# Performance work log

Measured on AMD Instinct MI355X. Metric: run time of the kernel, lower is better.

Reference implementation:

```python
import jax, jax.numpy as jnp
import numpy as np

B, TQ, TK, DQ, DK = 8, 2048, 2048, 512, 512


def setup_inputs() -> dict:
    key = jax.random.key(0)
    kq, kk, kv, km, kw = jax.random.split(key, 5)
    q = jax.random.normal(kq, (B, TQ, DQ), dtype=jnp.float32)
    k = jax.random.normal(kk, (B, TK, DK), dtype=jnp.float32)
    v = jax.random.normal(kv, (B, TK, DK), dtype=jnp.float32)
    attn_mask = jax.random.randint(km, (B, TQ, TK), 0, 2) > 0
    # xavier_uniform for (DQ, DK)
    limit = float(np.sqrt(6.0 / (DQ + DK)))
    weights = jax.random.uniform(kw, (DQ, DK), minval=-limit, maxval=limit, dtype=jnp.float32)
    return {"q": q, "k": k, "v": v, "attn_mask": attn_mask, "weights": weights}


def reference(q, k, v, attn_mask, weights):
    # scores: (B, TQ, TK) = (q @ W) @ k^T
    qw = jnp.einsum('bqd,de->bqe', q, weights)
    scores = jnp.einsum('bqe,bke->bqk', qw, k)
    scores = jnp.where(attn_mask, -jnp.inf, scores)
    attention = jax.nn.softmax(scores, axis=-1)
    # dropout_rate = 0.0 -> identity
    output = jnp.einsum('bqk,bkd->bqd', attention, v)
    return (output, attention)
```

## Files before the change

### kernel.cpp

```cpp
#include <hip/hip_runtime.h>
#include <stdint.h>

#define TQs 2048
#define TKs 2048
#define DDs 512
#define NBs 8

typedef float f32x4 __attribute__((ext_vector_type(4)));
typedef short bf16x8 __attribute__((ext_vector_type(8)));
typedef short bf16x4 __attribute__((ext_vector_type(4)));

__device__ __forceinline__ unsigned short f2bf(float x){
  unsigned u = __float_as_uint(x);
  return (unsigned short)((u + 0x7fffu + ((u>>16)&1u)) >> 16);
}
__device__ __forceinline__ float bf2f(unsigned short h){
  return __uint_as_float(((unsigned)h)<<16);
}

__device__ __forceinline__ void gload16(const void* g, void* l){
  __builtin_amdgcn_global_load_lds(
      (const __attribute__((address_space(1))) unsigned int*)(unsigned long long)(uintptr_t)g,
      (__attribute__((address_space(3))) unsigned int*)(unsigned int)(uintptr_t)l,
      16, 0, 0);
}

__global__ __launch_bounds__(256) void k0_split_k(const float* __restrict__ kk,
                                                  short* __restrict__ kh, short* __restrict__ kl){
  const long n4 = (long)NBs*TKs*DDs/4;
  for(long i = (long)blockIdx.x*256 + threadIdx.x; i < n4; i += (long)gridDim.x*256){
    f32x4 x = ((const f32x4*)kk)[i];
    bf16x4 h, l;
    #pragma unroll
    for(int j=0;j<4;j++){
      unsigned short hj = f2bf(x[j]);
      h[j] = (short)hj;
      l[j] = (short)f2bf(x[j] - bf2f(hj));
    }
    ((bf16x4*)kh)[i] = h;
    ((bf16x4*)kl)[i] = l;
  }
}

__global__ __launch_bounds__(256) void k0_transpose_v(const float* __restrict__ v, short* __restrict__ vt){
  __shared__ float tile[64][65];
  int b = blockIdx.z;
  int t0 = blockIdx.x*64, d0 = blockIdx.y*64;
  int tid = threadIdx.x;
  int r = tid>>2, cs = (tid&3)*16;
  const float* src = v + ((long)b*TKs + t0 + r)*DDs + d0 + cs;
  #pragma unroll
  for(int i=0;i<4;i++){
    f32x4 x = ((const f32x4*)src)[i];
    tile[r][cs+4*i+0]=x[0]; tile[r][cs+4*i+1]=x[1]; tile[r][cs+4*i+2]=x[2]; tile[r][cs+4*i+3]=x[3];
  }
  __syncthreads();
  int dr = tid>>2, ts = (tid&3)*16;
  bf16x8 b0, b1;
  #pragma unroll
  for(int i=0;i<8;i++){ b0[i] = (short)f2bf(tile[ts+i][dr]); b1[i] = (short)f2bf(tile[ts+8+i][dr]); }
  short* dst = vt + ((long)b*DDs + d0 + dr)*TKs + t0 + ts;
  ((bf16x8*)dst)[0] = b0;
  ((bf16x8*)dst)[1] = b1;
}

__global__ __launch_bounds__(256) void k0_wt(const float* __restrict__ wsrc,
                                             short* __restrict__ wth, short* __restrict__ wtl){
  __shared__ float tile[64][65];
  int d0 = blockIdx.x*64, e0 = blockIdx.y*64;
  int tid = threadIdx.x;
  int r = tid>>2, cs = (tid&3)*16;
  const float* src = wsrc + ((long)(d0 + r))*DDs + e0 + cs;
  #pragma unroll
  for(int i=0;i<4;i++){
    f32x4 x = ((const f32x4*)src)[i];
    tile[r][cs+4*i+0]=x[0]; tile[r][cs+4*i+1]=x[1]; tile[r][cs+4*i+2]=x[2]; tile[r][cs+4*i+3]=x[3];
  }
  __syncthreads();
  int er = tid>>2, ds = (tid&3)*16;
  bf16x8 h0,h1,l0,l1;
  #pragma unroll
  for(int i=0;i<8;i++){
    float x = tile[ds+i][er];
    unsigned short hh = f2bf(x);
    h0[i] = (short)hh; l0[i] = (short)f2bf(x - bf2f(hh));
  }
  #pragma unroll
  for(int i=0;i<8;i++){
    float x = tile[ds+8+i][er];
    unsigned short hh = f2bf(x);
    h1[i] = (short)hh; l1[i] = (short)f2bf(x - bf2f(hh));
  }
  short* dh = wth + ((long)(e0+er))*DDs + d0 + ds;
  short* dl = wtl + ((long)(e0+er))*DDs + d0 + ds;
  ((bf16x8*)dh)[0] = h0; ((bf16x8*)dh)[1] = h1;
  ((bf16x8*)dl)[0] = l0; ((bf16x8*)dl)[1] = l1;
}

__global__ __launch_bounds__(256,2) void k1_qw(const float* __restrict__ q,
                                               const short* __restrict__ wth, const short* __restrict__ wtl,
                                               short* __restrict__ qwh, short* __restrict__ qwl){
  __shared__ short qah[8192], qal[8192];
  __shared__ short wbh[8192], wbl[8192];
  int q0 = blockIdx.x*128, e0 = blockIdx.y*128;
  int tid = threadIdx.x, lane = tid&63, w4 = tid>>6;
  int wm = w4>>1, wn = w4&1;
  int i15 = lane&15, g4 = lane>>4;
  f32x4 acc[4][4];
  #pragma unroll
  for(int a=0;a<4;a++)
    #pragma unroll
    for(int bq=0;bq<4;bq++) acc[a][bq] = (f32x4){0.f,0.f,0.f,0.f};
  for(int k0=0;k0<DDs;k0+=64){
    __syncthreads();
    #pragma unroll
    for(int j=0;j<4;j++){
      int J = j*4 + w4;
      long so = (long)(e0 + (J>>1)*16 + i15)*DDs + k0 + ((J&1)*4 + g4)*8;
      gload16(wth + so, &wbh[J*512]);
      gload16(wtl + so, &wbl[J*512]);
    }
    #pragma unroll
    for(int j=0;j<4;j++){
      int c = j*256 + tid;
      int ci = c&15, cg = (c>>4)&3, cks = (c>>6)&1, crb = c>>7;
      const float* s = q + (long)(q0 + crb*16 + ci)*DDs + k0 + (cks*4+cg)*8;
      f32x4 x0 = ((const f32x4*)s)[0];
      f32x4 x1 = ((const f32x4*)s)[1];
      bf16x8 h, l;
      #pragma unroll
      for(int jj=0;jj<4;jj++){
        unsigned short hj = f2bf(x0[jj]);
        h[jj] = (short)hj; l[jj] = (short)f2bf(x0[jj]-bf2f(hj));
      }
      #pragma unroll
      for(int jj=0;jj<4;jj++){
        unsigned short hj = f2bf(x1[jj]);
        h[4+jj] = (short)hj; l[4+jj] = (short)f2bf(x1[jj]-bf2f(hj));
      }
      *(bf16x8*)&qah[c*8] = h;
      *(bf16x8*)&qal[c*8] = l;
    }
    __syncthreads();
    #pragma unroll
    for(int ks=0;ks<2;ks++){
      bf16x8 a_h[4], a_l[4], b_h[4], b_l[4];
      #pragma unroll
      for(int mf=0;mf<4;mf++){
        int c = ((wm*4+mf)*2+ks)*64 + lane;
        a_h[mf] = *(const bf16x8*)&qah[c*8];
        a_l[mf] = *(const bf16x8*)&qal[c*8];
      }
      #pragma unroll
      for(int nf=0;nf<4;nf++){
        int c = ((wn*4+nf)*2+ks)*64 + lane;
        b_h[nf] = *(const bf16x8*)&wbh[c*8];
        b_l[nf] = *(const bf16x8*)&wbl[c*8];
      }
      #pragma unroll
      for(int mf=0;mf<4;mf++)
      #pragma unroll
      for(int nf=0;nf<4;nf++){
        acc[mf][nf] = __builtin_amdgcn_mfma_f32_16x16x32_bf16(a_h[mf], b_h[nf], acc[mf][nf],0,0,0);
        acc[mf][nf] = __builtin_amdgcn_mfma_f32_16x16x32_bf16(a_h[mf], b_l[nf], acc[mf][nf],0,0,0);
        acc[mf][nf] = __builtin_amdgcn_mfma_f32_16x16x32_bf16(a_l[mf], b_h[nf], acc[mf][nf],0,0,0);
      }
    }
  }
  int rr = g4*4, cc = i15;
  #pragma unroll
  for(int mf=0;mf<4;mf++)
  #pragma unroll
  for(int nf=0;nf<4;nf++)
  #pragma unroll
  for(int r2=0;r2<4;r2++){
    long row = q0 + wm*64 + mf*16 + rr + r2;
    long col = e0 + wn*64 + nf*16 + cc;
    float s = acc[mf][nf][r2];
    unsigned short h = f2bf(s);
    qwh[row*DDs + col] = (short)h;
    qwl[row*DDs + col] = (short)f2bf(s - bf2f(h));
  }
}

__global__ __launch_bounds__(256,2) void k2a(const short* __restrict__ qwh, const short* __restrict__ qwl,
                                             const short* __restrict__ kh, const short* __restrict__ kl,
                                             const int* __restrict__ mask, float* __restrict__ attn,
                                             float* __restrict__ m_ws, float* __restrict__ l_ws){
  __shared__ short kfh[16384];
  __shared__ short kfl[16384];
  int rb = blockIdx.x;
  int chunk = blockIdx.y;
  int tid = threadIdx.x, lane = tid&63, w = tid>>6;
  int b = rb>>5;
  long qrow0 = (long)rb*64 + w*16;
  int i15 = lane&15, g4 = lane>>4;
  bf16x8 ah[16], al[16];
  {
    const short* ph = qwh + (qrow0 + i15)*DDs + g4*8;
    const short* pl = qwl + (qrow0 + i15)*DDs + g4*8;
    #pragma unroll
    for(int kc=0;kc<16;kc++){
      ah[kc] = *(const bf16x8*)(ph + kc*32);
      al[kc] = *(const bf16x8*)(pl + kc*32);
    }
  }
  float m_st[4], l_st[4];
  #pragma unroll
  for(int r=0;r<4;r++){ m_st[r]=-1e30f; l_st[r]=0.f; }
  const short* khb = kh + (long)b*TKs*DDs;
  const short* klb = kl + (long)b*TKs*DDs;
  for(int it=0; it<16; ++it){
    int t0 = chunk*512 + it*32;
    __syncthreads();
    #pragma unroll
    for(int j=0;j<8;j++){
      int J = j*4 + w;
      long so = (long)(t0 + ((J>>4)<<4) + i15)*DDs + ((J&15)*4 + g4)*8;
      gload16(khb + so, &kfh[J*512]);
      gload16(klb + so, &kfl[J*512]);
    }
    int mv[2][4];
    #pragma unroll
    for(int nf=0;nf<2;nf++)
      #pragma unroll
      for(int r=0;r<4;r++)
        mv[nf][r] = mask[(qrow0 + g4*4 + r)*TKs + t0 + nf*16 + i15];
    __syncthreads();
    f32x4 acc[2][3];
    #pragma unroll
    for(int nf=0;nf<2;nf++)
      #pragma unroll
      for(int c=0;c<3;c++) acc[nf][c]=(f32x4){0.f,0.f,0.f,0.f};
    #pragma unroll
    for(int ks=0;ks<16;ks++){
      #pragma unroll
      for(int nf=0;nf<2;nf++){
        bf16x8 bh = *(const bf16x8*)&kfh[((nf*16+ks)*64 + lane)*8];
        bf16x8 bl = *(const bf16x8*)&kfl[((nf*16+ks)*64 + lane)*8];
        acc[nf][0] = __builtin_amdgcn_mfma_f32_16x16x32_bf16(ah[ks], bh, acc[nf][0],0,0,0);
        acc[nf][1] = __builtin_amdgcn_mfma_f32_16x16x32_bf16(ah[ks], bl, acc[nf][1],0,0,0);
        acc[nf][2] = __builtin_amdgcn_mfma_f32_16x16x32_bf16(al[ks], bh, acc[nf][2],0,0,0);
      }
    }
    #pragma unroll
    for(int r=0;r<4;r++){
      float s0 = acc[0][0][r] + acc[0][1][r] + acc[0][2][r];
      float s1 = acc[1][0][r] + acc[1][1][r] + acc[1][2][r];
      if(mv[0][r]) s0 = -3e38f;
      if(mv[1][r]) s1 = -3e38f;
      float mx = fmaxf(s0,s1);
      #pragma unroll
      for(int d=1; d<16; d<<=1) mx = fmaxf(mx, __shfl_xor(mx, d, 16));
      float mold = m_st[r];
      float mnew = fmaxf(mold, mx);
      float p = __expf(s0-mnew) + __expf(s1-mnew);
      #pragma unroll
      for(int d=1; d<16; d<<=1) p += __shfl_xor(p, d, 16);
      l_st[r] = l_st[r]*__expf(mold-mnew) + p;
      m_st[r] = mnew;
      long row = qrow0 + g4*4 + r;
      attn[row*TKs + t0 + i15] = s0;
      attn[row*TKs + t0 + 16 + i15] = s1;
    }
  }
  if(i15==0){
    #pragma unroll
    for(int r=0;r<4;r++){
      long row = qrow0 + g4*4 + r;
      m_ws[row*4 + chunk] = m_st[r];
      l_ws[row*4 + chunk] = l_st[r];
    }
  }
}

__global__ __launch_bounds__(256,2) void k2b(const short* __restrict__ vt, const float* __restrict__ m_ws,
                                             const float* __restrict__ l_ws, float* __restrict__ attn,
                                             float* __restrict__ outp){
  __shared__ short vf[16384];
  __shared__ short at[2048];
  __shared__ float ms[64], rls[64];
  int rb = blockIdx.x;
  long row0 = (long)rb*64;
  int b = rb>>5;
  int tid=threadIdx.x, lane=tid&63, w=tid>>6;
  int i15 = lane&15, g4 = lane>>4;
  if(tid < 64){
    long row = row0 + tid;
    float m0=m_ws[row*4+0], m1=m_ws[row*4+1], m2=m_ws[row*4+2], m3=m_ws[row*4+3];
    float M = fmaxf(fmaxf(m0,m1),fmaxf(m2,m3));
    float L = l_ws[row*4+0]*__expf(m0-M) + l_ws[row*4+1]*__expf(m1-M)
            + l_ws[row*4+2]*__expf(m2-M) + l_ws[row*4+3]*__expf(m3-M);
    ms[tid] = M;
    rls[tid] = 1.0f/L;
  }
  f32x4 acc[4][8];
  #pragma unroll
  for(int mf=0;mf<4;mf++)
    #pragma unroll
    for(int nf=0;nf<8;nf++) acc[mf][nf]=(f32x4){0.f,0.f,0.f,0.f};
  const short* vb = vt + (long)b*DDs*TKs;
  float* arow = attn + row0*TKs;
  int r_ = tid>>2, t8w = tid&3;
  __syncthreads();
  for(int it=0; it<64; ++it){
    int t0 = it*32;
    #pragma unroll
    for(int j=0;j<8;j++){
      int J = j*4 + w;
      long so = (long)(J*16 + i15)*TKs + t0 + g4*8;
      gload16(vb + so, &vf[J*512]);
    }
    {
      float* p = arow + (long)r_*TKs + t0 + t8w*8;
      f32x4 s0v = ((const f32x4*)p)[0];
      f32x4 s1v = ((const f32x4*)p)[1];
      float M = ms[r_], RL = rls[r_];
      f32x4 a0, a1;
      #pragma unroll
      for(int j=0;j<4;j++){ a0[j] = __expf(s0v[j]-M)*RL; a1[j] = __expf(s1v[j]-M)*RL; }
      ((f32x4*)p)[0] = a0;
      ((f32x4*)p)[1] = a1;
      bf16x8 ab;
      #pragma unroll
      for(int j=0;j<4;j++){ ab[j] = (short)f2bf(a0[j]); ab[4+j] = (short)f2bf(a1[j]); }
      int cell = ((r_>>4)<<6) + (t8w<<4) + (r_&15);
      *(bf16x8*)&at[cell*8] = ab;
    }
    __syncthreads();
    bf16x8 af[4], bfr[8];
    #pragma unroll
    for(int mf=0;mf<4;mf++) af[mf] = *(const bf16x8*)&at[(mf*64 + lane)*8];
    #pragma unroll
    for(int nf=0;nf<8;nf++) bfr[nf] = *(const bf16x8*)&vf[((w*8+nf)*64 + lane)*8];
    #pragma unroll
    for(int mf=0;mf<4;mf++)
    #pragma unroll
    for(int nf=0;nf<8;nf++)
      acc[mf][nf] = __builtin_amdgcn_mfma_f32_16x16x32_bf16(af[mf], bfr[nf], acc[mf][nf],0,0,0);
    __syncthreads();
  }
  #pragma unroll
  for(int mf=0;mf<4;mf++)
  #pragma unroll
  for(int nf=0;nf<8;nf++)
  #pragma unroll
  for(int r2=0;r2<4;r2++){
    long row = row0 + mf*16 + g4*4 + r2;
    long col = w*128 + nf*16 + i15;
    outp[row*DDs + col] = acc[mf][nf][r2];
  }
}

extern "C" void kernel_launch(void* const* d_in, const int* in_sizes, int n_in,
                              void* d_out, int out_size, void* d_ws, size_t ws_size,
                              hipStream_t stream) {
  const float* q    = (const float*)d_in[0];
  const float* k    = (const float*)d_in[1];
  const float* v    = (const float*)d_in[2];
  const int*   mask = (const int*)d_in[3];
  const float* wsrc = (const float*)d_in[4];
  float* outp = (float*)d_out;
  float* attn = (float*)d_out + (long)NBs*TQs*DDs;
  char* ws = (char*)d_ws;
  const long NE = (long)NBs*TKs*DDs;
  short* kh  = (short*)ws;
  short* kl  = (short*)(ws + 2*NE);
  short* vt  = (short*)(ws + 4*NE);
  short* qwh = (short*)(ws + 6*NE);
  short* qwl = (short*)(ws + 8*NE);
  float* m_ws = (float*)(ws + 10*NE);
  float* l_ws = (float*)(ws + 10*NE + 65536*4);
  short* wth = (short*)attn;
  short* wtl = (short*)attn + 262144;
  hipLaunchKernelGGL(k0_split_k,     dim3(1024),    dim3(256), 0, stream, k, kh, kl);
  hipLaunchKernelGGL(k0_transpose_v, dim3(32,8,8),  dim3(256), 0, stream, v, vt);
  hipLaunchKernelGGL(k0_wt,          dim3(8,8),     dim3(256), 0, stream, wsrc, wth, wtl);
  hipLaunchKernelGGL(k1_qw,          dim3(128,4),   dim3(256), 0, stream, q, wth, wtl, qwh, qwl);
  hipLaunchKernelGGL(k2a,            dim3(256,4),   dim3(256), 0, stream, qwh, qwl, kh, kl, mask, attn, m_ws, l_ws);
  hipLaunchKernelGGL(k2b,            dim3(256),     dim3(256), 0, stream, vt, m_ws, l_ws, attn, outp);
}
```

Baseline: 399.8 us.

## Use fp16 split-precision for QK scores and double-buffer K and V tiles

Replaces the bf16 hi/lo three-MFMA score product with fp16. Q·W is stored as an fp16 hi/lo pair and K as a single fp16 value, so each score needs two MFMAs and K traffic is halved. The score kernel and the PV kernel now double-buffer their LDS tiles, prefetching the next tile while computing on the current one. Per-tile max/sum shuffles are replaced by per-lane online softmax statistics merged once at the end. fp16 narrows the exponent range and drops K's low-order bits, which risks accuracy, and the extra LDS buffers may reduce occupancy.

```diff
diff --git a/kernel.cpp b/kernel.cpp
--- a/kernel.cpp
+++ b/kernel.cpp
@@ -9,6 +9,7 @@
 typedef float f32x4 __attribute__((ext_vector_type(4)));
 typedef short bf16x8 __attribute__((ext_vector_type(8)));
 typedef short bf16x4 __attribute__((ext_vector_type(4)));
+typedef _Float16 half8 __attribute__((ext_vector_type(8)));
 
 __device__ __forceinline__ unsigned short f2bf(float x){
   unsigned u = __float_as_uint(x);
@@ -25,20 +26,15 @@
       16, 0, 0);
 }
 
-__global__ __launch_bounds__(256) void k0_split_k(const float* __restrict__ kk,
-                                                  short* __restrict__ kh, short* __restrict__ kl){
-  const long n4 = (long)NBs*TKs*DDs/4;
-  for(long i = (long)blockIdx.x*256 + threadIdx.x; i < n4; i += (long)gridDim.x*256){
-    f32x4 x = ((const f32x4*)kk)[i];
-    bf16x4 h, l;
-    #pragma unroll
-    for(int j=0;j<4;j++){
-      unsigned short hj = f2bf(x[j]);
-      h[j] = (short)hj;
-      l[j] = (short)f2bf(x[j] - bf2f(hj));
-    }
-    ((bf16x4*)kh)[i] = h;
-    ((bf16x4*)kl)[i] = l;
+__global__ __launch_bounds__(256) void k0_kf(const float* __restrict__ kk, _Float16* __restrict__ kf){
+  const long n8 = (long)NBs*TKs*DDs/8;
+  for(long i = (long)blockIdx.x*256 + threadIdx.x; i < n8; i += (long)gridDim.x*256){
+    f32x4 x0 = ((const f32x4*)kk)[2*i];
+    f32x4 x1 = ((const f32x4*)kk)[2*i+1];
+    half8 h;
+    #pragma unroll
+    for(int j=0;j<4;j++){ h[j] = (_Float16)x0[j]; h[4+j] = (_Float16)x1[j]; }
+    ((half8*)kf)[i] = h;
   }
 }
 
@@ -99,7 +95,7 @@
 
 __global__ __launch_bounds__(256,2) void k1_qw(const float* __restrict__ q,
                                                const short* __restrict__ wth, const short* __restrict__ wtl,
-                                               short* __restrict__ qwh, short* __restrict__ qwl){
+                                               _Float16* __restrict__ qwh, _Float16* __restrict__ qwl){
   __shared__ short qah[8192], qal[8192];
   __shared__ short wbh[8192], wbl[8192];
   int q0 = blockIdx.x*128, e0 = blockIdx.y*128;
@@ -177,48 +173,58 @@
     long row = q0 + wm*64 + mf*16 + rr + r2;
     long col = e0 + wn*64 + nf*16 + cc;
     float s = acc[mf][nf][r2];
-    unsigned short h = f2bf(s);
-    qwh[row*DDs + col] = (short)h;
-    qwl[row*DDs + col] = (short)f2bf(s - bf2f(h));
-  }
-}
-
-__global__ __launch_bounds__(256,2) void k2a(const short* __restrict__ qwh, const short* __restrict__ qwl,
-                                             const short* __restrict__ kh, const short* __restrict__ kl,
+    _Float16 h = (_Float16)s;
+    qwh[row*DDs + col] = h;
+    qwl[row*DDs + col] = (_Float16)(s - (float)h);
+  }
+}
+
+__global__ __launch_bounds__(256,2) void k2a(const _Float16* __restrict__ qwh, const _Float16* __restrict__ qwl,
+                                             const _Float16* __restrict__ kf,
                                              const int* __restrict__ mask, float* __restrict__ attn,
                                              float* __restrict__ m_ws, float* __restrict__ l_ws){
-  __shared__ short kfh[16384];
-  __shared__ short kfl[16384];
+  __shared__ _Float16 kb[2][16384];
   int rb = blockIdx.x;
   int chunk = blockIdx.y;
   int tid = threadIdx.x, lane = tid&63, w = tid>>6;
   int b = rb>>5;
   long qrow0 = (long)rb*64 + w*16;
   int i15 = lane&15, g4 = lane>>4;
-  bf16x8 ah[16], al[16];
+  half8 ah[16], al[16];
   {
-    const short* ph = qwh + (qrow0 + i15)*DDs + g4*8;
-    const short* pl = qwl + (qrow0 + i15)*DDs + g4*8;
+    const _Float16* ph = qwh + (qrow0 + i15)*DDs + g4*8;
+    const _Float16* pl = qwl + (qrow0 + i15)*DDs + g4*8;
     #pragma unroll
     for(int kc=0;kc<16;kc++){
-      ah[kc] = *(const bf16x8*)(ph + kc*32);
-      al[kc] = *(const bf16x8*)(pl + kc*32);
+      ah[kc] = *(const half8*)(ph + kc*32);
+      al[kc] = *(const half8*)(pl + kc*32);
     }
   }
   float m_st[4], l_st[4];
   #pragma unroll
   for(int r=0;r<4;r++){ m_st[r]=-1e30f; l_st[r]=0.f; }
-  const short* khb = kh + (long)b*TKs*DDs;
-  const short* klb = kl + (long)b*TKs*DDs;
+  const _Float16* kbase = kf + (long)b*TKs*DDs;
+  {
+    int t0 = chunk*512;
+    #pragma unroll
+    for(int j=0;j<8;j++){
+      int J = j*4 + w;
+      long so = (long)(t0 + ((J>>4)<<4) + i15)*DDs + (J&15)*32 + g4*8;
+      gload16(kbase + so, &kb[0][J*512]);
+    }
+  }
+  __syncthreads();
+  int cur = 0;
   for(int it=0; it<16; ++it){
     int t0 = chunk*512 + it*32;
-    __syncthreads();
-    #pragma unroll
-    for(int j=0;j<8;j++){
-      int J = j*4 + w;
-      long so = (long)(t0 + ((J>>4)<<4) + i15)*DDs + ((J&15)*4 + g4)*8;
-      gload16(khb + so, &kfh[J*512]);
-      gload16(klb + so, &kfl[J*512]);
+    if(it < 15){
+      int t1 = t0 + 32;
+      #pragma unroll
+      for(int j=0;j<8;j++){
+        int J = j*4 + w;
+        long so = (long)(t1 + ((J>>4)<<4) + i15)*DDs + (J&15)*32 + g4*8;
+        gload16(kbase + so, &kb[cur^1][J*512]);
+      }
     }
     int mv[2][4];
     #pragma unroll
@@ -226,42 +232,43 @@
       #pragma unroll
       for(int r=0;r<4;r++)
         mv[nf][r] = mask[(qrow0 + g4*4 + r)*TKs + t0 + nf*16 + i15];
-    __syncthreads();
-    f32x4 acc[2][3];
-    #pragma unroll
-    for(int nf=0;nf<2;nf++)
-      #pragma unroll
-      for(int c=0;c<3;c++) acc[nf][c]=(f32x4){0.f,0.f,0.f,0.f};
+    f32x4 acc[2];
+    acc[0]=(f32x4){0.f,0.f,0.f,0.f}; acc[1]=(f32x4){0.f,0.f,0.f,0.f};
     #pragma unroll
     for(int ks=0;ks<16;ks++){
       #pragma unroll
       for(int nf=0;nf<2;nf++){
-        bf16x8 bh = *(const bf16x8*)&kfh[((nf*16+ks)*64 + lane)*8];
-        bf16x8 bl = *(const bf16x8*)&kfl[((nf*16+ks)*64 + lane)*8];
-        acc[nf][0] = __builtin_amdgcn_mfma_f32_16x16x32_bf16(ah[ks], bh, acc[nf][0],0,0,0);
-        acc[nf][1] = __builtin_amdgcn_mfma_f32_16x16x32_bf16(ah[ks], bl, acc[nf][1],0,0,0);
-        acc[nf][2] = __builtin_amdgcn_mfma_f32_16x16x32_bf16(al[ks], bh, acc[nf][2],0,0,0);
+        half8 bh = *(const half8*)&kb[cur][((nf*16+ks)*64 + lane)*8];
+        acc[nf] = __builtin_amdgcn_mfma_f32_16x16x32_f16(ah[ks], bh, acc[nf],0,0,0);
+        acc[nf] = __builtin_amdgcn_mfma_f32_16x16x32_f16(al[ks], bh, acc[nf],0,0,0);
       }
     }
     #pragma unroll
     for(int r=0;r<4;r++){
-      float s0 = acc[0][0][r] + acc[0][1][r] + acc[0][2][r];
-      float s1 = acc[1][0][r] + acc[1][1][r] + acc[1][2][r];
+      float s0 = acc[0][r];
+      float s1 = acc[1][r];
       if(mv[0][r]) s0 = -3e38f;
       if(mv[1][r]) s1 = -3e38f;
-      float mx = fmaxf(s0,s1);
-      #pragma unroll
-      for(int d=1; d<16; d<<=1) mx = fmaxf(mx, __shfl_xor(mx, d, 16));
-      float mold = m_st[r];
-      float mnew = fmaxf(mold, mx);
-      float p = __expf(s0-mnew) + __expf(s1-mnew);
-      #pragma unroll
-      for(int d=1; d<16; d<<=1) p += __shfl_xor(p, d, 16);
-      l_st[r] = l_st[r]*__expf(mold-mnew) + p;
-      m_st[r] = mnew;
+      float mo = m_st[r];
+      float mn = fmaxf(mo, fmaxf(s0,s1));
+      l_st[r] = l_st[r]*__expf(mo-mn) + __expf(s0-mn) + __expf(s1-mn);
+      m_st[r] = mn;
       long row = qrow0 + g4*4 + r;
       attn[row*TKs + t0 + i15] = s0;
       attn[row*TKs + t0 + 16 + i15] = s1;
+    }
+    __syncthreads();
+    cur ^= 1;
+  }
+  #pragma unroll
+  for(int r=0;r<4;r++){
+    #pragma unroll
+    for(int d=1; d<16; d<<=1){
+      float m2 = __shfl_xor(m_st[r], d, 16);
+      float l2 = __shfl_xor(l_st[r], d, 16);
+      float mn = fmaxf(m_st[r], m2);
+      l_st[r] = l_st[r]*__expf(m_st[r]-mn) + l2*__expf(m2-mn);
+      m_st[r] = mn;
     }
   }
   if(i15==0){
@@ -277,14 +284,23 @@
 __global__ __launch_bounds__(256,2) void k2b(const short* __restrict__ vt, const float* __restrict__ m_ws,
                                              const float* __restrict__ l_ws, float* __restrict__ attn,
                                              float* __restrict__ outp){
-  __shared__ short vf[16384];
-  __shared__ short at[2048];
+  __shared__ short vf[2][16384];
+  __shared__ short at2[2][2048];
   __shared__ float ms[64], rls[64];
   int rb = blockIdx.x;
   long row0 = (long)rb*64;
   int b = rb>>5;
   int tid=threadIdx.x, lane=tid&63, w=tid>>6;
   int i15 = lane&15, g4 = lane>>4;
+  const short* vb = vt + (long)b*DDs*TKs;
+  float* arow = attn + row0*TKs;
+  int r_ = tid>>2, t8w = tid&3;
+  #pragma unroll
+  for(int j=0;j<8;j++){
+    int J = j*4 + w;
+    long so = (long)(J*16 + i15)*TKs + g4*8;
+    gload16(vb + so, &vf[0][J*512]);
+  }
   if(tid < 64){
     long row = row0 + tid;
     float m0=m_ws[row*4+0], m1=m_ws[row*4+1], m2=m_ws[row*4+2], m3=m_ws[row*4+3];
@@ -294,27 +310,57 @@
     ms[tid] = M;
     rls[tid] = 1.0f/L;
   }
+  __syncthreads();
+  {
+    float* p = arow + (long)r_*TKs + t8w*8;
+    f32x4 s0v = ((const f32x4*)p)[0];
+    f32x4 s1v = ((const f32x4*)p)[1];
+    float M = ms[r_], RL = rls[r_];
+    f32x4 a0, a1;
+    #pragma unroll
+    for(int j=0;j<4;j++){ a0[j] = __expf(s0v[j]-M)*RL; a1[j] = __expf(s1v[j]-M)*RL; }
+    ((f32x4*)p)[0] = a0;
+    ((f32x4*)p)[1] = a1;
+    bf16x8 ab;
+    #pragma unroll
+    for(int j=0;j<4;j++){ ab[j] = (short)f2bf(a0[j]); ab[4+j] = (short)f2bf(a1[j]); }
+    int cell = ((r_>>4)<<6) + (t8w<<4) + (r_&15);
+    *(bf16x8*)&at2[0][cell*8] = ab;
+  }
+  __syncthreads();
   f32x4 acc[4][8];
   #pragma unroll
   for(int mf=0;mf<4;mf++)
     #pragma unroll
     for(int nf=0;nf<8;nf++) acc[mf][nf]=(f32x4){0.f,0.f,0.f,0.f};
-  const short* vb = vt + (long)b*DDs*TKs;
-  float* arow = attn + row0*TKs;
-  int r_ = tid>>2, t8w = tid&3;
-  __syncthreads();
+  int c = 0;
   for(int it=0; it<64; ++it){
-    int t0 = it*32;
-    #pragma unroll
-    for(int j=0;j<8;j++){
-      int J = j*4 + w;
-      long so = (long)(J*16 + i15)*TKs + t0 + g4*8;
-      gload16(vb + so, &vf[J*512]);
-    }
-    {
-      float* p = arow + (long)r_*TKs + t0 + t8w*8;
-      f32x4 s0v = ((const f32x4*)p)[0];
-      f32x4 s1v = ((const f32x4*)p)[1];
+    f32x4 s0v, s1v;
+    if(it < 63){
+      int t1 = (it+1)*32;
+      #pragma unroll
+      for(int j=0;j<8;j++){
+        int J = j*4 + w;
+        long so = (long)(J*16 + i15)*TKs + t1 + g4*8;
+        gload16(vb + so, &vf[c^1][J*512]);
+      }
+      float* p = arow + (long)r_*TKs + t1 + t8w*8;
+      s0v = ((const f32x4*)p)[0];
+      s1v = ((const f32x4*)p)[1];
+    }
+    bf16x8 af[4], bfr[8];
+    #pragma unroll
+    for(int mf=0;mf<4;mf++) af[mf] = *(const bf16x8*)&at2[c][(mf*64 + lane)*8];
+    #pragma unroll
+    for(int nf=0;nf<8;nf++) bfr[nf] = *(const bf16x8*)&vf[c][((w*8+nf)*64 + lane)*8];
+    #pragma unroll
+    for(int mf=0;mf<4;mf++)
+    #pragma unroll
+    for(int nf=0;nf<8;nf++)
+      acc[mf][nf] = __builtin_amdgcn_mfma_f32_16x16x32_bf16(af[mf], bfr[nf], acc[mf][nf],0,0,0);
+    if(it < 63){
+      int t1 = (it+1)*32;
+      float* p = arow + (long)r_*TKs + t1 + t8w*8;
       float M = ms[r_], RL = rls[r_];
       f32x4 a0, a1;
       #pragma unroll
@@ -325,20 +371,10 @@
       #pragma unroll
       for(int j=0;j<4;j++){ ab[j] = (short)f2bf(a0[j]); ab[4+j] = (short)f2bf(a1[j]); }
       int cell = ((r_>>4)<<6) + (t8w<<4) + (r_&15);
-      *(bf16x8*)&at[cell*8] = ab;
+      *(bf16x8*)&at2[c^1][cell*8] = ab;
     }
     __syncthreads();
-    bf16x8 af[4], bfr[8];
-    #pragma unroll
-    for(int mf=0;mf<4;mf++) af[mf] = *(const bf16x8*)&at[(mf*64 + lane)*8];
-    #pragma unroll
-    for(int nf=0;nf<8;nf++) bfr[nf] = *(const bf16x8*)&vf[((w*8+nf)*64 + lane)*8];
-    #pragma unroll
-    for(int mf=0;mf<4;mf++)
-    #pragma unroll
-    for(int nf=0;nf<8;nf++)
-      acc[mf][nf] = __builtin_amdgcn_mfma_f32_16x16x32_bf16(af[mf], bfr[nf], acc[mf][nf],0,0,0);
-    __syncthreads();
+    c ^= 1;
   }
   #pragma unroll
   for(int mf=0;mf<4;mf++)
@@ -364,19 +400,18 @@
   float* attn = (float*)d_out + (long)NBs*TQs*DDs;
   char* ws = (char*)d_ws;
   const long NE = (long)NBs*TKs*DDs;
-  short* kh  = (short*)ws;
-  short* kl  = (short*)(ws + 2*NE);
-  short* vt  = (short*)(ws + 4*NE);
-  short* qwh = (short*)(ws + 6*NE);
-  short* qwl = (short*)(ws + 8*NE);
-  float* m_ws = (float*)(ws + 10*NE);
-  float* l_ws = (float*)(ws + 10*NE + 65536*4);
+  _Float16* kf  = (_Float16*)ws;
+  short*    vt  = (short*)(ws + 2*NE);
+  _Float16* qwh = (_Float16*)(ws + 4*NE);
+  _Float16* qwl = (_Float16*)(ws + 6*NE);
+  float* m_ws = (float*)(ws + 8*NE);
+  float* l_ws = (float*)(ws + 8*NE + 65536*4);
   short* wth = (short*)attn;
   short* wtl = (short*)attn + 262144;
-  hipLaunchKernelGGL(k0_split_k,     dim3(1024),    dim3(256), 0, stream, k, kh, kl);
+  hipLaunchKernelGGL(k0_kf,          dim3(1024),    dim3(256), 0, stream, k, kf);
   hipLaunchKernelGGL(k0_transpose_v, dim3(32,8,8),  dim3(256), 0, stream, v, vt);
   hipLaunchKernelGGL(k0_wt,          dim3(8,8),     dim3(256), 0, stream, wsrc, wth, wtl);
   hipLaunchKernelGGL(k1_qw,          dim3(128,4),   dim3(256), 0, stream, q, wth, wtl, qwh, qwl);
-  hipLaunchKernelGGL(k2a,            dim3(256,4),   dim3(256), 0, stream, qwh, qwl, kh, kl, mask, attn, m_ws, l_ws);
+  hipLaunchKernelGGL(k2a,            dim3(256,4),   dim3(256), 0, stream, qwh, qwl, kf, mask, attn, m_ws, l_ws);
   hipLaunchKernelGGL(k2b,            dim3(256),     dim3(256), 0, stream, vt, m_ws, l_ws, attn, outp);
 }
```

Result: faster. 321.1 us (-19.7%).
